# Performance work log

Measured on AMD Instinct MI355X. Metric: run time of the kernel, lower is better.

Reference implementation:

```python
import jax, jax.numpy as jnp
import numpy as np

BS, S, WIDTH, MODES = 2, 512, 64, 16
P = S * (S - 1) // 2
IU, JU = np.triu_indices(S, 1)  # upper-triangle (i<j) index constants
COLL_COEF = 0.9  # training=True path


def spectral_conv(x, w):
    # x: (bs, c_in, n), w: (c_in, c_out, modes, 2)
    n = x.shape[-1]
    xf = jnp.fft.rfft(x, axis=2, norm='ortho')  # (bs, c_in, n//2+1) complex
    wm = w[..., 0] + 1j * w[..., 1]
    out_m = jnp.einsum('bix,iox->box', xf[:, :, :MODES], wm)
    pad = jnp.zeros((x.shape[0], w.shape[1], n // 2 + 1 - MODES), dtype=out_m.dtype)
    return jnp.fft.irfft(jnp.concatenate([out_m, pad], axis=2), n=n, axis=2, norm='ortho')


def dsmc(x, a, rvec):
    # x, a: (bs, c, n); rvec: (bs, c, P) unit vectors along c.  dt=1, v = a*dt.
    bs, c, n = x.shape
    v = a
    x_r = jnp.linalg.norm(x[:, :, :, None] - x[:, :, None, :], axis=1)  # (bs, n, n)
    v_r = jnp.linalg.norm(v[:, :, :, None] - v[:, :, None, :], axis=1)
    v_cm = (v[:, :, :, None] + v[:, :, None, :]) * 0.5  # (bs, c, n, n)
    x_cm = (x[:, :, :, None] + x[:, :, None, :]) * 0.5
    u_x = jnp.exp(-x_r)
    v_r_max = jnp.max(v_r, axis=(1, 2), keepdims=True)  # (bs,1,1)
    mask = v_r / v_r_max * u_x
    cm = mask > (1.0 - COLL_COEF)  # collision mask (bs, n, n)
    # antisymmetric projection of v_r upper triangle onto random unit vectors
    proj = v_r[:, IU, JU][:, None, :] * rvec  # (bs, c, P)
    vrl = (jnp.zeros((bs, c, n, n), x.dtype)
           .at[:, :, IU, JU].set(proj)
           .at[:, :, JU, IU].set(-proj))
    delta_v = v_cm + vrl - v[:, :, :, None]
    cmf = cm.astype(x.dtype)
    v_new = v + jnp.sum(delta_v * cmf[:, None], axis=2)  # sum over partners i
    cmf = cmf + jnp.eye(n, dtype=x.dtype)[None]  # add self
    x_new = jnp.sum(x_cm * cmf[:, None], axis=2) / jnp.sum(cmf, axis=2)[:, None, :]
    x_new = x_new + v_new  # x = x + v*dt
    return x_new, v_new


def setup_inputs() -> dict:
    key = jax.random.key(0)
    ks = jax.random.split(key, 12)
    x = jax.random.normal(ks[0], (BS, S, 2), jnp.float32)
    v = jax.random.normal(ks[1], (BS, WIDTH, S), jnp.float32)
    vecs = jax.random.normal(ks[2], (4, BS, WIDTH, P), jnp.float32)
    vecs = vecs / jnp.linalg.norm(vecs, axis=2, keepdims=True)  # unit vectors over chnl
    fc0_w = jax.random.normal(ks[3], (2, WIDTH), jnp.float32) * 0.5
    fc0_b = jax.random.normal(ks[4], (WIDTH,), jnp.float32) * 0.1
    scale = 1.0 / (WIDTH * WIDTH)
    spec_w = jax.random.uniform(ks[5], (4, WIDTH, WIDTH, MODES, 2), jnp.float32) * scale
    conv_w = jax.random.normal(ks[6], (4, WIDTH, WIDTH), jnp.float32) * (WIDTH ** -0.5)
    conv_b = jax.random.normal(ks[7], (4, WIDTH), jnp.float32) * 0.05
    fc1_w = jax.random.normal(ks[8], (WIDTH, 128), jnp.float32) * (WIDTH ** -0.5)
    fc1_b = jnp.zeros((128,), jnp.float32)
    fc2_w = jax.random.normal(ks[9], (128, 1), jnp.float32) * (128 ** -0.5)
    fc2_b = jnp.zeros((1,), jnp.float32)
    return {"x": x, "v": v, "vecs": vecs, "fc0_w": fc0_w, "fc0_b": fc0_b,
            "spec_w": spec_w, "conv_w": conv_w, "conv_b": conv_b,
            "fc1_w": fc1_w, "fc1_b": fc1_b, "fc2_w": fc2_w, "fc2_b": fc2_b}


def reference(x, v, vecs, fc0_w, fc0_b, spec_w, conv_w, conv_b, fc1_w, fc1_b, fc2_w, fc2_b):
    # NOTE: v is overwritten by a*dt inside KINET_DSMC2 in the original; kept for signature fidelity.
    h = x @ fc0_w + fc0_b          # (bs, s, width)
    h = jnp.transpose(h, (0, 2, 1))  # (bs, width, s)
    for i in range(4):
        a = spectral_conv(h, spec_w[i])
        p = jnp.einsum('oi,bin->bon', conv_w[i], h) + conv_b[i][None, :, None]
        h, vv = dsmc(p, a, vecs[i])
        if i < 3:
            h = jax.nn.relu(h)
    h = jnp.transpose(h, (0, 2, 1))  # (bs, s, width)
    h = jax.nn.relu(h @ fc1_w + fc1_b)
    return h @ fc2_w + fc2_b  # (bs, s, 1)
```

## Files before the change

kernel.cpp:

```cpp
#include <hip/hip_runtime.h>
#include <math.h>

#define S 512
#define W 64
#define MODES 16
#define PAIRS 130816
#define INV_SQRT_N 0.04419417382415922f
#define TWO_PI_OVER_N 0.012271846303085130f

__global__ __launch_bounds__(256) void k_fft(const float* __restrict__ h,
                                             const float* __restrict__ x,
                                             const float* __restrict__ fc0w,
                                             const float* __restrict__ fc0b,
                                             float* __restrict__ Xf, int first) {
    int b = blockIdx.x >> 6, ch = blockIdx.x & 63;
    int tid = threadIdx.x;
    float v0, v1;
    if (first) {
        float w0 = fc0w[ch], w1 = fc0w[64 + ch], bb = fc0b[ch];
        const float* xb = x + (size_t)b * S * 2;
        v0 = xb[2 * tid] * w0 + xb[2 * tid + 1] * w1 + bb;
        v1 = xb[2 * (tid + 256)] * w0 + xb[2 * (tid + 256) + 1] * w1 + bb;
    } else {
        const float* hp = h + (b * W + ch) * S;
        v0 = hp[tid]; v1 = hp[tid + 256];
    }
    float re[MODES], im[MODES];
#pragma unroll
    for (int m = 0; m < MODES; ++m) {
        float sn, cs;
        sincosf(TWO_PI_OVER_N * (float)(m * tid), &sn, &cs);
        float a = (m & 1) ? (v0 - v1) : (v0 + v1);
        re[m] = a * cs;
        im[m] = -a * sn;
    }
    __shared__ float part[4][32];
    int lane = tid & 63, wv = tid >> 6;
#pragma unroll
    for (int m = 0; m < MODES; ++m) {
        float r = re[m], ii = im[m];
        for (int off = 32; off; off >>= 1) {
            r += __shfl_down(r, off);
            ii += __shfl_down(ii, off);
        }
        if (lane == 0) { part[wv][2 * m] = r; part[wv][2 * m + 1] = ii; }
    }
    __syncthreads();
    if (tid < 32) {
        float s = part[0][tid] + part[1][tid] + part[2][tid] + part[3][tid];
        Xf[(b * W + ch) * 32 + tid] = s * INV_SQRT_N;
    }
}

__global__ __launch_bounds__(256) void k_mix(const float* __restrict__ Xf,
                                             const float* __restrict__ specw,
                                             float* __restrict__ Y, int l) {
    int b = blockIdx.x >> 6, o = blockIdx.x & 63;
    int tid = threadIdx.x, m = tid & 15, ip = tid >> 4;
    __shared__ float Xs[2048];
    for (int idx = tid; idx < 2048; idx += 256) Xs[idx] = Xf[b * 2048 + idx];
    __syncthreads();
    float ar = 0.f, ai = 0.f;
#pragma unroll
    for (int q = 0; q < 4; ++q) {
        int i = ip * 4 + q;
        const float* wp = specw + (size_t)(((l * W + i) * W + o) * MODES + m) * 2;
        float wr = wp[0], wi = wp[1];
        float xr = Xs[i * 32 + 2 * m], xi = Xs[i * 32 + 2 * m + 1];
        ar += xr * wr - xi * wi;
        ai += xr * wi + xi * wr;
    }
    __shared__ float redr[16][17], redi[16][17];
    redr[ip][m] = ar; redi[ip][m] = ai;
    __syncthreads();
    if (tid < 16) {
        float sr = 0.f, si = 0.f;
        for (int p = 0; p < 16; ++p) { sr += redr[p][tid]; si += redi[p][tid]; }
        Y[(b * W + o) * 32 + 2 * tid] = sr;
        Y[(b * W + o) * 32 + 2 * tid + 1] = si;
    }
}

__global__ __launch_bounds__(256) void k_ac(const float* __restrict__ Y,
                                            const float* __restrict__ h,
                                            const float* __restrict__ x,
                                            const float* __restrict__ fc0w,
                                            const float* __restrict__ fc0b,
                                            const float* __restrict__ convw,
                                            const float* __restrict__ convb,
                                            float* __restrict__ aT,
                                            float* __restrict__ pT,
                                            unsigned* __restrict__ vmax,
                                            int l, int first) {
    int blk = blockIdx.x;
    int b = blk >> 7, t0 = (blk & 127) * 4;
    int tid = threadIdx.x;
    int o = tid & 63, tg = tid >> 6;
    if (blk == 0 && tid < 2) vmax[tid] = 0u;
    __shared__ float hs[64 * 5];
    {
        int r = tid >> 2, t = tid & 3;
        if (first) {
            const float* xb = x + ((size_t)b * S + t0 + t) * 2;
            hs[r * 5 + t] = xb[0] * fc0w[r] + xb[1] * fc0w[64 + r] + fc0b[r];
        } else {
            hs[r * 5 + t] = h[(b * W + r) * S + t0 + t];
        }
    }
    float yr[MODES], yi[MODES];
    const float4* yp = (const float4*)(Y + b * 2048 + o * 32);
#pragma unroll
    for (int q = 0; q < 8; ++q) {
        float4 y4 = yp[q];
        yr[2 * q] = y4.x; yi[2 * q] = y4.y;
        yr[2 * q + 1] = y4.z; yi[2 * q + 1] = y4.w;
    }
    int t = t0 + tg;
    float acc = yr[0];
#pragma unroll
    for (int m = 1; m < MODES; ++m) {
        float sn, cs;
        sincosf(TWO_PI_OVER_N * (float)(m * t), &sn, &cs);
        acc += 2.0f * (yr[m] * cs - yi[m] * sn);
    }
    aT[((size_t)b * S + t) * W + o] = acc * INV_SQRT_N;
    __syncthreads();
    float pacc = convb[l * W + o];
    const float4* wp = (const float4*)(convw + l * 4096 + o * 64);
#pragma unroll
    for (int i4 = 0; i4 < 16; ++i4) {
        float4 w4 = wp[i4];
        pacc = fmaf(w4.x, hs[(4 * i4 + 0) * 5 + tg], pacc);
        pacc = fmaf(w4.y, hs[(4 * i4 + 1) * 5 + tg], pacc);
        pacc = fmaf(w4.z, hs[(4 * i4 + 2) * 5 + tg], pacc);
        pacc = fmaf(w4.w, hs[(4 * i4 + 3) * 5 + tg], pacc);
    }
    pT[((size_t)b * S + t) * W + o] = pacc;
}

__global__ __launch_bounds__(256) void k_pair(const float* __restrict__ pT,
                                              const float* __restrict__ aT,
                                              float* __restrict__ vr,
                                              float* __restrict__ uxm,
                                              unsigned* __restrict__ vmax) {
    int blk = blockIdx.x;
    int b = blk >> 8;
    int rest = blk & 255;
    int i0 = (rest & 15) * 32, j0 = (rest >> 4) * 32;
    int tid = threadIdx.x;
    int tx = tid & 15, ty = tid >> 4;
    __shared__ float Pi[64 * 33], Pj[64 * 33], Vi[64 * 33], Vj[64 * 33];
    for (int idx = tid; idx < 2048; idx += 256) {
        int k = idx >> 6, c = idx & 63;
        Pi[c * 33 + k] = pT[(b * S + i0 + k) * W + c];
        Pj[c * 33 + k] = pT[(b * S + j0 + k) * W + c];
        Vi[c * 33 + k] = aT[(b * S + i0 + k) * W + c];
        Vj[c * 33 + k] = aT[(b * S + j0 + k) * W + c];
    }
    __syncthreads();
    float ax[2][2] = {{0.f, 0.f}, {0.f, 0.f}};
    float av[2][2] = {{0.f, 0.f}, {0.f, 0.f}};
    for (int c = 0; c < W; ++c) {
        float pi0 = Pi[c * 33 + 2 * tx], pi1 = Pi[c * 33 + 2 * tx + 1];
        float pj0 = Pj[c * 33 + 2 * ty], pj1 = Pj[c * 33 + 2 * ty + 1];
        float vi0 = Vi[c * 33 + 2 * tx], vi1 = Vi[c * 33 + 2 * tx + 1];
        float vj0 = Vj[c * 33 + 2 * ty], vj1 = Vj[c * 33 + 2 * ty + 1];
        float d;
        d = pi0 - pj0; ax[0][0] = fmaf(d, d, ax[0][0]);
        d = pi1 - pj0; ax[1][0] = fmaf(d, d, ax[1][0]);
        d = pi0 - pj1; ax[0][1] = fmaf(d, d, ax[0][1]);
        d = pi1 - pj1; ax[1][1] = fmaf(d, d, ax[1][1]);
        d = vi0 - vj0; av[0][0] = fmaf(d, d, av[0][0]);
        d = vi1 - vj0; av[1][0] = fmaf(d, d, av[1][0]);
        d = vi0 - vj1; av[0][1] = fmaf(d, d, av[0][1]);
        d = vi1 - vj1; av[1][1] = fmaf(d, d, av[1][1]);
    }
    float mx = 0.f;
#pragma unroll
    for (int jj = 0; jj < 2; ++jj) {
#pragma unroll
        for (int ii = 0; ii < 2; ++ii) {
            int i = i0 + 2 * tx + ii, j = j0 + 2 * ty + jj;
            float xr = sqrtf(ax[ii][jj]);
            float vv = sqrtf(av[ii][jj]);
            vr[((size_t)b * S + j) * S + i] = vv;
            uxm[((size_t)b * S + j) * S + i] = expf(-xr);
            mx = fmaxf(mx, vv);
        }
    }
    __shared__ float mxs[4];
    for (int off = 32; off; off >>= 1) mx = fmaxf(mx, __shfl_xor(mx, off));
    if ((tid & 63) == 0) mxs[tid >> 6] = mx;
    __syncthreads();
    if (tid == 0) {
        float m = fmaxf(fmaxf(mxs[0], mxs[1]), fmaxf(mxs[2], mxs[3]));
        atomicMax(&vmax[b], __float_as_uint(m));
    }
}

__global__ __launch_bounds__(256) void k_mpf(const float* __restrict__ vr,
                                             const float* __restrict__ uxm,
                                             const unsigned* __restrict__ vmaxu,
                                             const float* __restrict__ aT,
                                             const float* __restrict__ pT,
                                             const float* __restrict__ vecs,
                                             float* __restrict__ h_std,
                                             const float* __restrict__ fc1w,
                                             const float* __restrict__ fc1b,
                                             const float* __restrict__ fc2w,
                                             const float* __restrict__ fc2b,
                                             float* __restrict__ out,
                                             int l, int do_relu, int do_head) {
    int b = blockIdx.x >> 9, q = blockIdx.x & 511;
    int tid = threadIdx.x, lane = tid & 63, wv = tid >> 6;
    __shared__ float wrow[S];
    __shared__ float SV[4][64], SX[4][64], TP[4][64];
    __shared__ float hrow[64];
    __shared__ int cnt4[4];
    const float* vrp = vr + ((size_t)b * S + q) * S;
    const float* uxp = uxm + ((size_t)b * S + q) * S;
    float vmax = __uint_as_float(vmaxu[b]);
    int mycnt = 0;
    for (int i = tid; i < S; i += 256) {
        float v = vrp[i], u = uxp[i];
        bool act = (v / vmax) * u > 0.1f;
        wrow[i] = act ? v : 0.f;
        mycnt += act ? 1 : 0;
    }
    for (int o = 32; o; o >>= 1) mycnt += __shfl_down(mycnt, o);
    if (lane == 0) cnt4[wv] = mycnt;
    __syncthreads();
    float A = (float)(cnt4[0] + cnt4[1] + cnt4[2] + cnt4[3]);
    float svp = 0.f, sxp = 0.f, tp = 0.f;
    const float* aTb = aT + (size_t)b * S * W;
    const float* pTb = pT + (size_t)b * S * W;
    const float* Rb = vecs + (size_t)((l * 2 + b) * W + lane) * PAIRS;
    int triq = q * 511 - ((q * (q - 1)) >> 1);
    for (int k = 0; k < 128; ++k) {
        int p = wv * 128 + k;
        float w = wrow[p];
        if (w != 0.f) {
            svp += aTb[p * W + lane];
            sxp += pTb[p * W + lane];
            int idx; float sgn;
            if (p < q) { idx = p * 511 - ((p * (p - 1)) >> 1) + (q - p - 1); sgn = 1.f; }
            else       { idx = triq + (p - q - 1); sgn = -1.f; }
            tp = fmaf(sgn * w, Rb[idx], tp);
        }
    }
    SV[wv][lane] = svp; SX[wv][lane] = sxp; TP[wv][lane] = tp;
    __syncthreads();
    if (wv == 0) {
        float sv = SV[0][lane] + SV[1][lane] + SV[2][lane] + SV[3][lane];
        float sx = SX[0][lane] + SX[1][lane] + SX[2][lane] + SX[3][lane];
        float T  = TP[0][lane] + TP[1][lane] + TP[2][lane] + TP[3][lane];
        float vj = aTb[q * W + lane], xj = pTb[q * W + lane];
        float vnew = vj + 0.5f * (A * vj - sv) + T;
        float accx = 0.5f * (A * xj + sx);
        float xnew = (xj + accx) / (A + 1.0f) + vnew;
        if (do_relu) xnew = fmaxf(xnew, 0.0f);
        if (!do_head) h_std[((size_t)b * W + lane) * S + q] = xnew;
        else hrow[lane] = xnew;
    }
    if (do_head) {
        __syncthreads();
        if (wv == 0) {
            float a0 = fc1b[lane], a1 = fc1b[lane + 64];
            for (int cc = 0; cc < W; ++cc) {
                float hv = hrow[cc];
                a0 = fmaf(hv, fc1w[cc * 128 + lane], a0);
                a1 = fmaf(hv, fc1w[cc * 128 + lane + 64], a1);
            }
            a0 = fmaxf(a0, 0.f); a1 = fmaxf(a1, 0.f);
            float p = a0 * fc2w[lane] + a1 * fc2w[lane + 64];
            for (int off = 32; off; off >>= 1) p += __shfl_down(p, off);
            if (lane == 0) out[b * S + q] = p + fc2b[0];
        }
    }
}

extern "C" void kernel_launch(void* const* d_in, const int* in_sizes, int n_in,
                              void* d_out, int out_size, void* d_ws, size_t ws_size,
                              hipStream_t stream) {
    const float* x = (const float*)d_in[0];
    const float* vecs = (const float*)d_in[2];
    const float* fc0w = (const float*)d_in[3];
    const float* fc0b = (const float*)d_in[4];
    const float* specw = (const float*)d_in[5];
    const float* convw = (const float*)d_in[6];
    const float* convb = (const float*)d_in[7];
    const float* fc1w = (const float*)d_in[8];
    const float* fc1b = (const float*)d_in[9];
    const float* fc2w = (const float*)d_in[10];
    const float* fc2b = (const float*)d_in[11];
    float* out = (float*)d_out;

    char* ws = (char*)d_ws;
    unsigned* vmax = (unsigned*)ws;
    float* h_std = (float*)(ws + 256);
    float* aT = h_std + 65536;
    float* pT = aT + 65536;
    float* Xf = pT + 65536;
    float* Yb = Xf + 4096;
    float* vrbuf = Yb + 4096;
    float* uxbuf = vrbuf + 524288;

    for (int l = 0; l < 4; ++l) {
        int first = (l == 0) ? 1 : 0;
        k_fft<<<128, 256, 0, stream>>>(h_std, x, fc0w, fc0b, Xf, first);
        k_mix<<<128, 256, 0, stream>>>(Xf, specw, Yb, l);
        k_ac<<<256, 256, 0, stream>>>(Yb, h_std, x, fc0w, fc0b, convw, convb,
                                      aT, pT, vmax, l, first);
        k_pair<<<512, 256, 0, stream>>>(pT, aT, vrbuf, uxbuf, vmax);
        k_mpf<<<1024, 256, 0, stream>>>(vrbuf, uxbuf, vmax, aT, pT, vecs,
                                        h_std, fc1w, fc1b, fc2w, fc2b, out,
                                        l, (l < 3) ? 1 : 0, (l == 3) ? 1 : 0);
    }
}
```

Baseline: 655.9 us.

## Replace per-mode sincos with twiddle recurrence and vectorize shared/global loads

The forward and inverse truncated DFT kernels now compute one sincos per thread and step through the modes with a complex rotation recurrence, replacing one transcendental call per mode. The pair-distance kernel pads its shared tiles to stride 34 with 16-byte alignment so each thread can read float2 pairs instead of scalar loads. The collision kernel reads its row with a single float2 load per thread. The recurrence adds a little rounding drift over 16 steps, and the new shared-memory padding may change the bank-conflict pattern.

```diff
diff --git a/kernel.cpp b/kernel.cpp
--- a/kernel.cpp
+++ b/kernel.cpp
@@ -25,14 +25,19 @@
         const float* hp = h + (b * W + ch) * S;
         v0 = hp[tid]; v1 = hp[tid + 256];
     }
+    float c1, s1;
+    sincosf(TWO_PI_OVER_N * (float)tid, &s1, &c1);
+    float cm = 1.f, sm = 0.f;
+    float ap = v0 + v1, am = v0 - v1;
     float re[MODES], im[MODES];
 #pragma unroll
     for (int m = 0; m < MODES; ++m) {
-        float sn, cs;
-        sincosf(TWO_PI_OVER_N * (float)(m * tid), &sn, &cs);
-        float a = (m & 1) ? (v0 - v1) : (v0 + v1);
-        re[m] = a * cs;
-        im[m] = -a * sn;
+        float a = (m & 1) ? am : ap;
+        re[m] = a * cm;
+        im[m] = -a * sm;
+        float nc = cm * c1 - sm * s1;
+        float ns = sm * c1 + cm * s1;
+        cm = nc; sm = ns;
     }
     __shared__ float part[4][32];
     int lane = tid & 63, wv = tid >> 6;
@@ -116,12 +121,16 @@
         yr[2 * q + 1] = y4.z; yi[2 * q + 1] = y4.w;
     }
     int t = t0 + tg;
+    float c1, s1;
+    sincosf(TWO_PI_OVER_N * (float)t, &s1, &c1);
+    float cm = c1, sm = s1;
     float acc = yr[0];
 #pragma unroll
     for (int m = 1; m < MODES; ++m) {
-        float sn, cs;
-        sincosf(TWO_PI_OVER_N * (float)(m * t), &sn, &cs);
-        acc += 2.0f * (yr[m] * cs - yi[m] * sn);
+        acc += 2.0f * (yr[m] * cm - yi[m] * sm);
+        float nc = cm * c1 - sm * s1;
+        float ns = sm * c1 + cm * s1;
+        cm = nc; sm = ns;
     }
     aT[((size_t)b * S + t) * W + o] = acc * INV_SQRT_N;
     __syncthreads();
@@ -149,31 +158,34 @@
     int i0 = (rest & 15) * 32, j0 = (rest >> 4) * 32;
     int tid = threadIdx.x;
     int tx = tid & 15, ty = tid >> 4;
-    __shared__ float Pi[64 * 33], Pj[64 * 33], Vi[64 * 33], Vj[64 * 33];
+    __shared__ __align__(16) float Pi[64 * 34];
+    __shared__ __align__(16) float Pj[64 * 34];
+    __shared__ __align__(16) float Vi[64 * 34];
+    __shared__ __align__(16) float Vj[64 * 34];
     for (int idx = tid; idx < 2048; idx += 256) {
         int k = idx >> 6, c = idx & 63;
-        Pi[c * 33 + k] = pT[(b * S + i0 + k) * W + c];
-        Pj[c * 33 + k] = pT[(b * S + j0 + k) * W + c];
-        Vi[c * 33 + k] = aT[(b * S + i0 + k) * W + c];
-        Vj[c * 33 + k] = aT[(b * S + j0 + k) * W + c];
+        Pi[c * 34 + k] = pT[(b * S + i0 + k) * W + c];
+        Pj[c * 34 + k] = pT[(b * S + j0 + k) * W + c];
+        Vi[c * 34 + k] = aT[(b * S + i0 + k) * W + c];
+        Vj[c * 34 + k] = aT[(b * S + j0 + k) * W + c];
     }
     __syncthreads();
     float ax[2][2] = {{0.f, 0.f}, {0.f, 0.f}};
     float av[2][2] = {{0.f, 0.f}, {0.f, 0.f}};
     for (int c = 0; c < W; ++c) {
-        float pi0 = Pi[c * 33 + 2 * tx], pi1 = Pi[c * 33 + 2 * tx + 1];
-        float pj0 = Pj[c * 33 + 2 * ty], pj1 = Pj[c * 33 + 2 * ty + 1];
-        float vi0 = Vi[c * 33 + 2 * tx], vi1 = Vi[c * 33 + 2 * tx + 1];
-        float vj0 = Vj[c * 33 + 2 * ty], vj1 = Vj[c * 33 + 2 * ty + 1];
+        float2 pi = *(const float2*)&Pi[c * 34 + 2 * tx];
+        float2 pj = *(const float2*)&Pj[c * 34 + 2 * ty];
+        float2 vi = *(const float2*)&Vi[c * 34 + 2 * tx];
+        float2 vj = *(const float2*)&Vj[c * 34 + 2 * ty];
         float d;
-        d = pi0 - pj0; ax[0][0] = fmaf(d, d, ax[0][0]);
-        d = pi1 - pj0; ax[1][0] = fmaf(d, d, ax[1][0]);
-        d = pi0 - pj1; ax[0][1] = fmaf(d, d, ax[0][1]);
-        d = pi1 - pj1; ax[1][1] = fmaf(d, d, ax[1][1]);
-        d = vi0 - vj0; av[0][0] = fmaf(d, d, av[0][0]);
-        d = vi1 - vj0; av[1][0] = fmaf(d, d, av[1][0]);
-        d = vi0 - vj1; av[0][1] = fmaf(d, d, av[0][1]);
-        d = vi1 - vj1; av[1][1] = fmaf(d, d, av[1][1]);
+        d = pi.x - pj.x; ax[0][0] = fmaf(d, d, ax[0][0]);
+        d = pi.y - pj.x; ax[1][0] = fmaf(d, d, ax[1][0]);
+        d = pi.x - pj.y; ax[0][1] = fmaf(d, d, ax[0][1]);
+        d = pi.y - pj.y; ax[1][1] = fmaf(d, d, ax[1][1]);
+        d = vi.x - vj.x; av[0][0] = fmaf(d, d, av[0][0]);
+        d = vi.y - vj.x; av[1][0] = fmaf(d, d, av[1][0]);
+        d = vi.x - vj.y; av[0][1] = fmaf(d, d, av[0][1]);
+        d = vi.y - vj.y; av[1][1] = fmaf(d, d, av[1][1]);
     }
     float mx = 0.f;
 #pragma unroll
@@ -221,11 +233,14 @@
     const float* uxp = uxm + ((size_t)b * S + q) * S;
     float vmax = __uint_as_float(vmaxu[b]);
     int mycnt = 0;
-    for (int i = tid; i < S; i += 256) {
-        float v = vrp[i], u = uxp[i];
-        bool act = (v / vmax) * u > 0.1f;
-        wrow[i] = act ? v : 0.f;
-        mycnt += act ? 1 : 0;
+    {
+        float2 v2 = *(const float2*)&vrp[2 * tid];
+        float2 u2 = *(const float2*)&uxp[2 * tid];
+        bool a0 = (v2.x / vmax) * u2.x > 0.1f;
+        bool a1 = (v2.y / vmax) * u2.y > 0.1f;
+        wrow[2 * tid] = a0 ? v2.x : 0.f;
+        wrow[2 * tid + 1] = a1 ? v2.y : 0.f;
+        mycnt = (a0 ? 1 : 0) + (a1 ? 1 : 0);
     }
     for (int o = 32; o; o >>= 1) mycnt += __shfl_down(mycnt, o);
     if (lane == 0) cnt4[wv] = mycnt;
@@ -237,7 +252,7 @@
     const float* Rb = vecs + (size_t)((l * 2 + b) * W + lane) * PAIRS;
     int triq = q * 511 - ((q * (q - 1)) >> 1);
     for (int k = 0; k < 128; ++k) {
-        int p = wv * 128 + k;
+        int p = (wv << 7) + k;
         float w = wrow[p];
         if (w != 0.f) {
             svp += aTb[p * W + lane];
```

Result: no change. 651.4 us (-0.7%).
